# Performance work log

Measured on AMD Instinct MI355X. Metric: run time of the kernel, lower is better.

## Reference

```python
import jax, jax.numpy as jnp
import numpy as np

# Fixed problem sizes (equal-sized batch segments, matching setup_inputs)
B, N, M = 4, 4096, 16384          # clouds, coarse pts/cloud, fine pts/cloud
C_IN, C_SKIP, K = 256, 256, 3     # feature dims, knn k
CH = [C_IN + C_SKIP, 512, 256]    # MLP channels
EPS = 1e-16


def setup_inputs() -> dict:
    key = jax.random.key(0)
    ks = jax.random.split(key, 6)
    x = jax.random.normal(ks[0], (B * N, C_IN), jnp.float32)
    pos = jax.random.uniform(ks[1], (B * N, 3), jnp.float32)
    batch = jnp.repeat(jnp.arange(B, dtype=jnp.int64), N)
    x_skip = jax.random.normal(ks[2], (B * M, C_SKIP), jnp.float32)
    pos_skip = jax.random.uniform(ks[3], (B * M, 3), jnp.float32)
    batch_skip = jnp.repeat(jnp.arange(B, dtype=jnp.int64), M)
    W1 = jax.random.normal(ks[4], (CH[0], CH[1]), jnp.float32) / np.sqrt(CH[0]).astype(np.float32)
    b1 = jnp.zeros((CH[1],), jnp.float32)
    W2 = jax.random.normal(ks[5], (CH[1], CH[2]), jnp.float32) / np.sqrt(CH[1]).astype(np.float32)
    b2 = jnp.zeros((CH[2],), jnp.float32)
    return dict(x=x, pos=pos, batch=batch, x_skip=x_skip, pos_skip=pos_skip,
                batch_skip=batch_skip, W1=W1, b1=b1, W2=W2, b2=b2)


def _knn_interpolate(x, pos, pos_skip):
    """torch_geometric.nn.knn_interpolate with equal-sized batch segments."""
    xb = x.reshape(B, N, C_IN)
    ps = pos.reshape(B, N, 3)
    qs = pos_skip.reshape(B, M, 3)
    # squared pairwise distances [B, M, N]
    d2 = (jnp.sum(qs * qs, -1)[:, :, None]
          - 2.0 * jnp.einsum('bmd,bnd->bmn', qs, ps)
          + jnp.sum(ps * ps, -1)[:, None, :])
    neg_d2, idx = jax.lax.top_k(-d2, K)                # k smallest distances, [B,M,K]
    w = 1.0 / jnp.clip(-neg_d2, EPS)                   # inverse squared distance weights
    feats = jax.vmap(lambda f, i: f[i])(xb, idx)       # gather: [B, M, K, C_IN]
    y = jnp.sum(w[..., None] * feats, axis=2) / jnp.sum(w, axis=2)[..., None]
    return y.reshape(B * M, C_IN)


def reference(x, pos, batch, x_skip, pos_skip, batch_skip, W1, b1, W2, b2):
    y = _knn_interpolate(x, pos, pos_skip)
    h = jnp.concatenate([y, x_skip], axis=1)           # [B*M, 512]
    h = jax.nn.relu(h @ W1 + b1)
    h = jax.nn.relu(h @ W2 + b2)
    return h, pos_skip, batch_skip
```

## Files before the change

### kernel.cpp

```cpp
#include <hip/hip_runtime.h>
#include <stdint.h>

#define NB 4
#define NPTS 4096
#define MPTS 16384
#define CIN 256
#define CH0 512
#define CH1 512
#define CH2 256
#define ROWS (NB * MPTS)
#define POS_OUT_OFF (ROWS * CH2)
#define BATCH_OUT_OFF (POS_OUT_OFF + ROWS * 3)
#define CELL_CAP 40
#define QCAP 96

using u16 = unsigned short;
using u32 = unsigned int;
using u64 = unsigned long long;

typedef __bf16 bf16x8 __attribute__((ext_vector_type(8)));
typedef float f32x4 __attribute__((ext_vector_type(4)));

__device__ __forceinline__ u16 f2bf(float f) {
  u32 u = __builtin_bit_cast(u32, f);
  u32 r = u + 0x7fffu + ((u >> 16) & 1u);
  return (u16)(r >> 16);
}

__device__ __forceinline__ u32 flipf(float f) {
  u32 u = __builtin_bit_cast(u32, f);
  return u ^ ((u32)((int)u >> 31) | 0x80000000u);
}
__device__ __forceinline__ float unflipf(u32 f) {
  u32 m = (~(u32)((int)f >> 31)) | 0x80000000u;
  return __builtin_bit_cast(float, f ^ m);
}

__device__ __forceinline__ void ins3(u64 v, u64& k0, u64& k1, u64& k2) {
  u64 a = k0 < v ? v : k0;
  k0 = k0 < v ? k0 : v;
  u64 bb = k1 < a ? a : k1;
  k1 = k1 < a ? k1 : a;
  k2 = k2 < bb ? k2 : bb;
}

__device__ __forceinline__ void merge3(u64 r0, u64 r1, u64 r2,
                                       u64& k0, u64& k1, u64& k2) {
  u64 t = k0 < r0 ? r0 : k0;
  k0 = k0 < r0 ? k0 : r0;
  u64 u = k1 < r1 ? k1 : r1;
  u64 mtu = t < u ? u : t;
  k1 = t < u ? t : u;
  u64 v = k2 < r2 ? k2 : r2;
  k2 = mtu < v ? mtu : v;
}

__device__ __forceinline__ u64 shfl_xor_u64_w8(u64 v, int mask) {
  u32 lo = (u32)v, hi = (u32)(v >> 32);
  lo = (u32)__shfl_xor((int)lo, mask, 8);
  hi = (u32)__shfl_xor((int)hi, mask, 8);
  return ((u64)hi << 32) | lo;
}

__global__ __launch_bounds__(256) void prep_kernel(
    const float* __restrict__ W1, const float* __restrict__ W2,
    u16* __restrict__ W1s, u16* __restrict__ W2s) {
  const int t = blockIdx.x * 256 + threadIdx.x;
  if (t < 32768) {
    const int l = t & 63, ni = (t >> 6) & 3, wd = (t >> 8) & 7, kt = t >> 11;
    const int fr = l & 15, g = l >> 4;
    const int n = wd * 64 + ni * 16 + fr;
    u16 o[8];
#pragma unroll
    for (int j = 0; j < 8; ++j)
      o[j] = f2bf(W1[(kt * 32 + g * 8 + j) * CH1 + n]);
    *(uint4*)(W1s + (size_t)t * 8) = *(const uint4*)o;
  } else {
    const int c = t - 32768;
    const int l = c & 63, ni = (c >> 6) & 1, wd = (c >> 7) & 7, kt = c >> 10;
    const int fr = l & 15, g = l >> 4;
    const int n = wd * 32 + ni * 16 + fr;
    u16 o[8];
#pragma unroll
    for (int j = 0; j < 8; ++j)
      o[j] = f2bf(W2[(kt * 32 + g * 8 + j) * CH2 + n]);
    *(uint4*)(W2s + (size_t)c * 8) = *(const uint4*)o;
  }
}

__global__ __launch_bounds__(256) void tail_kernel(
    const float* __restrict__ pos_skip, const int* __restrict__ batch_skip,
    float* __restrict__ out) {
  int t = blockIdx.x * 256 + threadIdx.x;
  if (t < ROWS * 3) {
    out[POS_OUT_OFF + t] = pos_skip[t];
  } else {
    int u = t - ROWS * 3;
    out[BATCH_OUT_OFF + u] = (float)batch_skip[u];
  }
}

__global__ __launch_bounds__(256) void build_kernel(
    const float* __restrict__ pos, float4* __restrict__ pts4,
    u32* __restrict__ cellCnt, int* __restrict__ cellIdx) {
#pragma clang fp contract(off)
  const int i = blockIdx.x * 256 + threadIdx.x;
  const float x = pos[i * 3 + 0], y = pos[i * 3 + 1], z = pos[i * 3 + 2];
  pts4[i] = make_float4(x, y, z, (x * x + y * y) + z * z);
  const int b = i >> 12;
  int cx = (int)(x * 8.0f); cx = cx < 0 ? 0 : (cx > 7 ? 7 : cx);
  int cy = (int)(y * 8.0f); cy = cy < 0 ? 0 : (cy > 7 ? 7 : cy);
  int cz = (int)(z * 8.0f); cz = cz < 0 ? 0 : (cz > 7 ? 7 : cz);
  const int c = b * 512 + cz * 64 + cy * 8 + cx;
  const u32 slot = atomicAdd(&cellCnt[c], 1u);
  if (slot < CELL_CAP) cellIdx[c * CELL_CAP + slot] = i;
}

__global__ __launch_bounds__(256) void qbin_kernel(
    const float* __restrict__ pos_skip, u32* __restrict__ qCnt,
    int* __restrict__ qIdx) {
  const int q = blockIdx.x * 256 + threadIdx.x;
  const int b = q >> 14;
  const float qx = pos_skip[q * 3 + 0];
  const float qy = pos_skip[q * 3 + 1];
  const float qz = pos_skip[q * 3 + 2];
  int cx = (int)(qx * 8.0f); cx = cx < 0 ? 0 : (cx > 7 ? 7 : cx);
  int cy = (int)(qy * 8.0f); cy = cy < 0 ? 0 : (cy > 7 ? 7 : cy);
  int cz = (int)(qz * 8.0f); cz = cz < 0 ? 0 : (cz > 7 ? 7 : cz);
  const int c = b * 512 + cz * 64 + cy * 8 + cx;
  const u32 slot = atomicAdd(&qCnt[c], 1u);
  if (slot < QCAP) qIdx[c * QCAP + slot] = q;
}

__global__ __launch_bounds__(256) void knn_kernel(
    const float4* __restrict__ pts4, const u32* __restrict__ cellCnt,
    const int* __restrict__ cellIdx, const u32* __restrict__ qCnt,
    const int* __restrict__ qIdx, const float* __restrict__ pos_skip,
    int* __restrict__ idx_out, float* __restrict__ w_out) {
#pragma clang fp contract(off)
  __shared__ float4 scand[27 * CELL_CAP];
  __shared__ int    scgi[27 * CELL_CAP];
  __shared__ u32    scnt[27];
  __shared__ int    sbase[27];
  __shared__ u32    nCand;
  const int tid = threadIdx.x;
  const int b = blockIdx.x >> 9;
  const int cell = blockIdx.x & 511;
  const int cz = cell >> 6, cy = (cell >> 3) & 7, cx = cell & 7;
  const int x0 = cx > 0 ? cx - 1 : 0, x1 = cx < 7 ? cx + 1 : 7;
  const int y0 = cy > 0 ? cy - 1 : 0, y1 = cy < 7 ? cy + 1 : 7;
  const int z0 = cz > 0 ? cz - 1 : 0, z1 = cz < 7 ? cz + 1 : 7;
  const int nx = x1 - x0 + 1, ny = y1 - y0 + 1, nz = z1 - z0 + 1;
  const int ncells = nx * ny * nz;
  if (tid == 0) nCand = 0;
  if (tid < ncells) {
    const int lz = tid / (nx * ny);
    const int rem = tid - lz * nx * ny;
    const int ly = rem / nx;
    const int lx = rem - ly * nx;
    const int cg = b * 512 + (z0 + lz) * 64 + (y0 + ly) * 8 + (x0 + lx);
    u32 cnt = cellCnt[cg];
    scnt[tid] = cnt > CELL_CAP ? CELL_CAP : cnt;
    sbase[tid] = cg * CELL_CAP;
  }
  __syncthreads();
  const int slots = ncells * CELL_CAP;
  for (int s = tid; s < slots; s += 256) {
    const int ci = s / CELL_CAP;
    const int sl = s - ci * CELL_CAP;
    if ((u32)sl < scnt[ci]) {
      const int gi = cellIdx[sbase[ci] + sl];
      const float4 p = pts4[gi];
      const u32 d = atomicAdd(&nCand, 1u);
      scand[d] = p;
      scgi[d] = gi;
    }
  }
  __syncthreads();
  const int nC = (int)nCand;
  u32 nq = qCnt[b * 512 + cell];
  if (nq > QCAP) nq = QCAP;
  const int qbase = (b * 512 + cell) * QCAP;
  const int g = tid >> 3;
  const int sub = tid & 7;

  for (int r0q = 0; r0q < (int)nq; r0q += 32) {
    const int qslot = r0q + g;
    if (qslot < (int)nq) {
      const int q = qIdx[qbase + qslot];
      const float qx = pos_skip[q * 3 + 0];
      const float qy = pos_skip[q * 3 + 1];
      const float qz = pos_skip[q * 3 + 2];
      const float q2 = (qx * qx + qy * qy) + qz * qz;
      u64 k0 = ~0ull, k1 = ~0ull, k2 = ~0ull;
      for (int s = sub; s < nC; s += 8) {
        const float4 p = scand[s];
        const float dot = fmaf(qz, p.z, fmaf(qy, p.y, qx * p.x));
        const float tv = (q2 - 2.0f * dot) + p.w;
        const u64 key = ((u64)flipf(tv) << 32) | (u32)scgi[s];
        ins3(key, k0, k1, k2);
      }
#pragma unroll
      for (int mask = 1; mask < 8; mask <<= 1) {
        const u64 r0 = shfl_xor_u64_w8(k0, mask);
        const u64 r1 = shfl_xor_u64_w8(k1, mask);
        const u64 r2 = shfl_xor_u64_w8(k2, mask);
        merge3(r0, r1, r2, k0, k1, k2);
      }
      float m2tv = unflipf((u32)(k2 >> 32));
      if (!(m2tv <= 0.015625f - 1e-5f)) {
        k0 = k1 = k2 = ~0ull;
        const int ex0 = cx > 1 ? cx - 2 : 0, ex1 = cx < 6 ? cx + 2 : 7;
        const int ey0 = cy > 1 ? cy - 2 : 0, ey1 = cy < 6 ? cy + 2 : 7;
        const int ez0 = cz > 1 ? cz - 2 : 0, ez1 = cz < 6 ? cz + 2 : 7;
        for (int zz = ez0; zz <= ez1; ++zz)
          for (int yy = ey0; yy <= ey1; ++yy)
            for (int xx = ex0; xx <= ex1; ++xx) {
              const int cg = b * 512 + zz * 64 + yy * 8 + xx;
              u32 cnt = cellCnt[cg];
              if (cnt > CELL_CAP) cnt = CELL_CAP;
              const int cb = cg * CELL_CAP;
              for (int s = sub; s < (int)cnt; s += 8) {
                const int gi = cellIdx[cb + s];
                const float4 p = pts4[gi];
                const float dot = fmaf(qz, p.z, fmaf(qy, p.y, qx * p.x));
                const float tv = (q2 - 2.0f * dot) + p.w;
                ins3(((u64)flipf(tv) << 32) | (u32)gi, k0, k1, k2);
              }
            }
#pragma unroll
        for (int mask = 1; mask < 8; mask <<= 1) {
          const u64 r0 = shfl_xor_u64_w8(k0, mask);
          const u64 r1 = shfl_xor_u64_w8(k1, mask);
          const u64 r2 = shfl_xor_u64_w8(k2, mask);
          merge3(r0, r1, r2, k0, k1, k2);
        }
        m2tv = unflipf((u32)(k2 >> 32));
        if (!(m2tv <= 0.0625f - 1e-5f)) {
          k0 = k1 = k2 = ~0ull;
          const int base = b * NPTS;
          for (int i = sub; i < NPTS; i += 8) {
            const int gi = base + i;
            const float4 p = pts4[gi];
            const float dot = fmaf(qz, p.z, fmaf(qy, p.y, qx * p.x));
            const float tv = (q2 - 2.0f * dot) + p.w;
            ins3(((u64)flipf(tv) << 32) | (u32)gi, k0, k1, k2);
          }
#pragma unroll
          for (int mask = 1; mask < 8; mask <<= 1) {
            const u64 r0 = shfl_xor_u64_w8(k0, mask);
            const u64 r1 = shfl_xor_u64_w8(k1, mask);
            const u64 r2 = shfl_xor_u64_w8(k2, mask);
            merge3(r0, r1, r2, k0, k1, k2);
          }
        }
      }
      if (sub == 0) {
        const float t0 = unflipf((u32)(k0 >> 32));
        const float t1 = unflipf((u32)(k1 >> 32));
        const float t2 = unflipf((u32)(k2 >> 32));
        const float w0 = 1.0f / fmaxf(t0, 1e-16f);
        const float w1 = 1.0f / fmaxf(t1, 1e-16f);
        const float w2 = 1.0f / fmaxf(t2, 1e-16f);
        const float wsum = (w0 + w1) + w2;
        const float inv = 1.0f / wsum;
        idx_out[q * 3 + 0] = (int)(u32)k0;
        idx_out[q * 3 + 1] = (int)(u32)k1;
        idx_out[q * 3 + 2] = (int)(u32)k2;
        w_out[q * 3 + 0] = w0 * inv;
        w_out[q * 3 + 1] = w1 * inv;
        w_out[q * 3 + 2] = w2 * inv;
      }
    }
  }
}

__global__ __launch_bounds__(512, 2) void fused_mlp_kernel(
    const float* __restrict__ x, const int* __restrict__ idx,
    const float* __restrict__ w, const float* __restrict__ x_skip,
    const u16* __restrict__ W1s, const float* __restrict__ b1,
    const u16* __restrict__ W2s, const float* __restrict__ b2,
    float* __restrict__ out) {
  __shared__ __align__(16) u16 Abuf[64 * 512];
  const int tid = threadIdx.x;
  const int m0 = blockIdx.x * 64;

  {
    const int row = tid >> 3;
    const int sub = tid & 7;
    const int gr = m0 + row;
    u16* rowp = Abuf + row * 512;
    const int rx = row & 7;
    if (sub < 4) {
      const int i0 = idx[gr * 3 + 0], i1 = idx[gr * 3 + 1], i2 = idx[gr * 3 + 2];
      const float w0 = w[gr * 3 + 0], w1 = w[gr * 3 + 1], w2 = w[gr * 3 + 2];
      const float4* p0 = (const float4*)(x + (size_t)i0 * CIN + sub * 64);
      const float4* p1 = (const float4*)(x + (size_t)i1 * CIN + sub * 64);
      const float4* p2 = (const float4*)(x + (size_t)i2 * CIN + sub * 64);
#pragma unroll
      for (int c = 0; c < 8; ++c) {
        const float4 a0 = p0[c * 2], a1 = p1[c * 2], a2 = p2[c * 2];
        const float4 d0 = p0[c * 2 + 1], d1 = p1[c * 2 + 1], d2 = p2[c * 2 + 1];
        u16 o[8];
        o[0] = f2bf(fmaf(w0, a0.x, fmaf(w1, a1.x, w2 * a2.x)));
        o[1] = f2bf(fmaf(w0, a0.y, fmaf(w1, a1.y, w2 * a2.y)));
        o[2] = f2bf(fmaf(w0, a0.z, fmaf(w1, a1.z, w2 * a2.z)));
        o[3] = f2bf(fmaf(w0, a0.w, fmaf(w1, a1.w, w2 * a2.w)));
        o[4] = f2bf(fmaf(w0, d0.x, fmaf(w1, d1.x, w2 * d2.x)));
        o[5] = f2bf(fmaf(w0, d0.y, fmaf(w1, d1.y, w2 * d2.y)));
        o[6] = f2bf(fmaf(w0, d0.z, fmaf(w1, d1.z, w2 * d2.z)));
        o[7] = f2bf(fmaf(w0, d0.w, fmaf(w1, d1.w, w2 * d2.w)));
        const int vg = sub * 8 + c;
        *(uint4*)(rowp + (vg ^ rx) * 8) = *(const uint4*)o;
      }
    } else {
      const float4* ps = (const float4*)(x_skip + (size_t)gr * CIN + (sub - 4) * 64);
#pragma unroll
      for (int c = 0; c < 8; ++c) {
        const float4 a = ps[c * 2], d = ps[c * 2 + 1];
        u16 o[8];
        o[0] = f2bf(a.x); o[1] = f2bf(a.y); o[2] = f2bf(a.z); o[3] = f2bf(a.w);
        o[4] = f2bf(d.x); o[5] = f2bf(d.y); o[6] = f2bf(d.z); o[7] = f2bf(d.w);
        const int vg = 32 + (sub - 4) * 8 + c;
        *(uint4*)(rowp + (vg ^ rx) * 8) = *(const uint4*)o;
      }
    }
  }
  __syncthreads();

  const int wid = tid >> 6;
  const int lane = tid & 63;
  const int fr = lane & 15;
  const int g = lane >> 4;
  const int frx = fr & 7;

  f32x4 acc[4][4];
#pragma unroll
  for (int mi = 0; mi < 4; mi++)
#pragma unroll
    for (int ni = 0; ni < 4; ni++) acc[mi][ni] = (f32x4){0.f, 0.f, 0.f, 0.f};

  {
    const u16* B1 = W1s + wid * 2048 + lane * 8;
    bf16x8 bf[2][4];
#pragma unroll
    for (int ni = 0; ni < 4; ni++)
      bf[0][ni] = *(const bf16x8*)(B1 + ni * 512);
    for (int kt = 0; kt < 16; ++kt) {
      const int cur = kt & 1;
      if (kt < 15) {
        const u16* nb = B1 + (kt + 1) * 16384;
#pragma unroll
        for (int ni = 0; ni < 4; ni++)
          bf[cur ^ 1][ni] = *(const bf16x8*)(nb + ni * 512);
      }
      bf16x8 af[4];
#pragma unroll
      for (int mi = 0; mi < 4; mi++)
        af[mi] = *(const bf16x8*)&Abuf[(mi * 16 + fr) * 512 +
                                       (((kt * 4 + g) ^ frx) * 8)];
#pragma unroll
      for (int mi = 0; mi < 4; mi++)
#pragma unroll
        for (int ni = 0; ni < 4; ni++)
          acc[mi][ni] = __builtin_amdgcn_mfma_f32_16x16x32_bf16(
              af[mi], bf[cur][ni], acc[mi][ni], 0, 0, 0);
    }
  }
  __syncthreads();

  {
    const int wn = wid * 64;
#pragma unroll
    for (int ni = 0; ni < 4; ni++) {
      const int n = wn + ni * 16 + fr;
      const float bb = b1[n];
      const int vg = n >> 3;
      const int nlow = n & 7;
#pragma unroll
      for (int mi = 0; mi < 4; mi++) {
#pragma unroll
        for (int r = 0; r < 4; r++) {
          const int m = mi * 16 + g * 4 + r;
          const float v = fmaxf(acc[mi][ni][r] + bb, 0.f);
          Abuf[m * 512 + (vg ^ (m & 7)) * 8 + nlow] = f2bf(v);
        }
      }
    }
  }
  __syncthreads();

  f32x4 acc2[4][2];
#pragma unroll
  for (int mi = 0; mi < 4; mi++)
#pragma unroll
    for (int ni = 0; ni < 2; ni++) acc2[mi][ni] = (f32x4){0.f, 0.f, 0.f, 0.f};

  {
    const u16* B2 = W2s + wid * 1024 + lane * 8;
    bf16x8 bf[2][2];
#pragma unroll
    for (int ni = 0; ni < 2; ni++)
      bf[0][ni] = *(const bf16x8*)(B2 + ni * 512);
    for (int kt = 0; kt < 16; ++kt) {
      const int cur = kt & 1;
      if (kt < 15) {
        const u16* nb = B2 + (kt + 1) * 8192;
#pragma unroll
        for (int ni = 0; ni < 2; ni++)
          bf[cur ^ 1][ni] = *(const bf16x8*)(nb + ni * 512);
      }
      bf16x8 af[4];
#pragma unroll
      for (int mi = 0; mi < 4; mi++)
        af[mi] = *(const bf16x8*)&Abuf[(mi * 16 + fr) * 512 +
                                       (((kt * 4 + g) ^ frx) * 8)];
#pragma unroll
      for (int mi = 0; mi < 4; mi++)
#pragma unroll
        for (int ni = 0; ni < 2; ni++)
          acc2[mi][ni] = __builtin_amdgcn_mfma_f32_16x16x32_bf16(
              af[mi], bf[cur][ni], acc2[mi][ni], 0, 0, 0);
    }
  }

#pragma unroll
  for (int ni = 0; ni < 2; ni++) {
    const int col = wid * 32 + ni * 16 + fr;
    const float bb = b2[col];
#pragma unroll
    for (int mi = 0; mi < 4; mi++) {
#pragma unroll
      for (int r = 0; r < 4; r++) {
        const int rowg = m0 + mi * 16 + g * 4 + r;
        out[(size_t)rowg * CH2 + col] = fmaxf(acc2[mi][ni][r] + bb, 0.f);
      }
    }
  }
}

extern "C" void kernel_launch(void* const* d_in, const int* in_sizes, int n_in,
                              void* d_out, int out_size, void* d_ws, size_t ws_size,
                              hipStream_t stream) {
  const float* x        = (const float*)d_in[0];
  const float* pos      = (const float*)d_in[1];
  const float* x_skip   = (const float*)d_in[3];
  const float* pos_skip = (const float*)d_in[4];
  const int*   batch_sk = (const int*)d_in[5];
  const float* W1       = (const float*)d_in[6];
  const float* b1       = (const float*)d_in[7];
  const float* W2       = (const float*)d_in[8];
  const float* b2       = (const float*)d_in[9];
  float* out = (float*)d_out;

  char* ws = (char*)d_ws;
  u16*    W1s     = (u16*)(ws);
  u16*    W2s     = (u16*)(ws + 524288);
  int*    idxb    = (int*)(ws + 786432);
  float*  wb      = (float*)(ws + 1572864);
  float4* pts4    = (float4*)(ws + 2359296);
  u32*    cellCnt = (u32*)(ws + 2621440);
  u32*    qCnt    = (u32*)(ws + 2629632);
  int*    cellIdx = (int*)(ws + 2637824);
  int*    qIdx    = (int*)(ws + 2965504);

  hipMemsetAsync(cellCnt, 0, 16384, stream);
  prep_kernel<<<dim3(192), dim3(256), 0, stream>>>(W1, W2, W1s, W2s);
  tail_kernel<<<dim3(1024), dim3(256), 0, stream>>>(pos_skip, batch_sk, out);
  build_kernel<<<dim3(64), dim3(256), 0, stream>>>(pos, pts4, cellCnt, cellIdx);
  qbin_kernel<<<dim3(256), dim3(256), 0, stream>>>(pos_skip, qCnt, qIdx);
  knn_kernel<<<dim3(2048), dim3(256), 0, stream>>>(pts4, cellCnt, cellIdx,
                                                   qCnt, qIdx, pos_skip,
                                                   idxb, wb);
  fused_mlp_kernel<<<dim3(1024), dim3(512), 0, stream>>>(
      x, idxb, wb, x_skip, W1s, b1, W2s, b2, out);
}
```

Baseline: 272.0 us.

## Swap MFMA operand roles, split layer-1 N into two passes, raise occupancy

Swaps the MFMA operands so weights are the A operand and activations the B operand. Each lane's accumulator then holds four consecutive output columns, which allows packed 8-byte LDS stores for the hidden layer and float4 global stores for the output. Layer 1 now runs in two passes of half the N width, with the first pass's bf16 results packed into registers. This cuts accumulator registers so launch bounds can rise to 4 blocks per CU. The cost is re-reading the A tiles from LDS in each pass, and occupancy is still capped by the 64 KB shared buffer per block.

New measurement: 280.8 us. 3.2% more time.

```diff
diff --git a/kernel.cpp b/kernel.cpp
--- a/kernel.cpp
+++ b/kernel.cpp
@@ -275,7 +275,7 @@
   }
 }
 
-__global__ __launch_bounds__(512, 2) void fused_mlp_kernel(
+__global__ __launch_bounds__(512, 4) void fused_mlp_kernel(
     const float* __restrict__ x, const int* __restrict__ idx,
     const float* __restrict__ w, const float* __restrict__ x_skip,
     const u16* __restrict__ W1s, const float* __restrict__ b1,
@@ -334,107 +334,133 @@
   const int g = lane >> 4;
   const int frx = fr & 7;
 
-  f32x4 acc[4][4];
-#pragma unroll
-  for (int mi = 0; mi < 4; mi++)
-#pragma unroll
-    for (int ni = 0; ni < 4; ni++) acc[mi][ni] = (f32x4){0.f, 0.f, 0.f, 0.f};
-
-  {
-    const u16* B1 = W1s + wid * 2048 + lane * 8;
-    bf16x8 bf[2][4];
-#pragma unroll
-    for (int ni = 0; ni < 4; ni++)
-      bf[0][ni] = *(const bf16x8*)(B1 + ni * 512);
+  f32x4 acc[2][4];
+  u32 hold[16];
+#pragma unroll
+  for (int p = 0; p < 2; ++p) {
+#pragma unroll
+    for (int mi = 0; mi < 2; mi++)
+#pragma unroll
+      for (int ni = 0; ni < 4; ni++) acc[mi][ni] = (f32x4){0.f, 0.f, 0.f, 0.f};
+    const u16* B1 = W1s + wid * 2048 + (p * 2) * 512 + lane * 8;
+    bf16x8 bw[2][2];
+#pragma unroll
+    for (int i = 0; i < 2; i++) bw[0][i] = *(const bf16x8*)(B1 + i * 512);
     for (int kt = 0; kt < 16; ++kt) {
       const int cur = kt & 1;
       if (kt < 15) {
         const u16* nb = B1 + (kt + 1) * 16384;
 #pragma unroll
-        for (int ni = 0; ni < 4; ni++)
-          bf[cur ^ 1][ni] = *(const bf16x8*)(nb + ni * 512);
+        for (int i = 0; i < 2; i++)
+          bw[cur ^ 1][i] = *(const bf16x8*)(nb + i * 512);
       }
       bf16x8 af[4];
 #pragma unroll
-      for (int mi = 0; mi < 4; mi++)
-        af[mi] = *(const bf16x8*)&Abuf[(mi * 16 + fr) * 512 +
+      for (int ni = 0; ni < 4; ni++)
+        af[ni] = *(const bf16x8*)&Abuf[(ni * 16 + fr) * 512 +
                                        (((kt * 4 + g) ^ frx) * 8)];
 #pragma unroll
-      for (int mi = 0; mi < 4; mi++)
+      for (int mi = 0; mi < 2; mi++)
 #pragma unroll
         for (int ni = 0; ni < 4; ni++)
           acc[mi][ni] = __builtin_amdgcn_mfma_f32_16x16x32_bf16(
-              af[mi], bf[cur][ni], acc[mi][ni], 0, 0, 0);
+              bw[cur][mi], af[ni], acc[mi][ni], 0, 0, 0);
+    }
+    if (p == 0) {
+#pragma unroll
+      for (int mi = 0; mi < 2; mi++) {
+        const int cb = wid * 64 + mi * 16 + g * 4;
+        const float4 bv = *(const float4*)&b1[cb];
+#pragma unroll
+        for (int ni = 0; ni < 4; ni++) {
+          const u16 t0 = f2bf(fmaxf(acc[mi][ni][0] + bv.x, 0.f));
+          const u16 t1 = f2bf(fmaxf(acc[mi][ni][1] + bv.y, 0.f));
+          const u16 t2 = f2bf(fmaxf(acc[mi][ni][2] + bv.z, 0.f));
+          const u16 t3 = f2bf(fmaxf(acc[mi][ni][3] + bv.w, 0.f));
+          hold[(mi * 4 + ni) * 2 + 0] = (u32)t0 | ((u32)t1 << 16);
+          hold[(mi * 4 + ni) * 2 + 1] = (u32)t2 | ((u32)t3 << 16);
+        }
+      }
     }
   }
   __syncthreads();
 
-  {
-    const int wn = wid * 64;
-#pragma unroll
-    for (int ni = 0; ni < 4; ni++) {
-      const int n = wn + ni * 16 + fr;
-      const float bb = b1[n];
-      const int vg = n >> 3;
-      const int nlow = n & 7;
-#pragma unroll
-      for (int mi = 0; mi < 4; mi++) {
-#pragma unroll
-        for (int r = 0; r < 4; r++) {
-          const int m = mi * 16 + g * 4 + r;
-          const float v = fmaxf(acc[mi][ni][r] + bb, 0.f);
-          Abuf[m * 512 + (vg ^ (m & 7)) * 8 + nlow] = f2bf(v);
-        }
+#pragma unroll
+  for (int mi = 0; mi < 2; mi++) {
+    {
+      const int cb = wid * 64 + mi * 16 + g * 4;
+      const int vg = cb >> 3, cl = cb & 7;
+#pragma unroll
+      for (int ni = 0; ni < 4; ni++) {
+        const int row = ni * 16 + fr;
+        uint2 pk = make_uint2(hold[(mi * 4 + ni) * 2 + 0],
+                              hold[(mi * 4 + ni) * 2 + 1]);
+        *(uint2*)&Abuf[row * 512 + (vg ^ (row & 7)) * 8 + cl] = pk;
+      }
+    }
+    {
+      const int cb = wid * 64 + 32 + mi * 16 + g * 4;
+      const float4 bv = *(const float4*)&b1[cb];
+      const int vg = cb >> 3, cl = cb & 7;
+#pragma unroll
+      for (int ni = 0; ni < 4; ni++) {
+        const int row = ni * 16 + fr;
+        uint2 pk;
+        pk.x = (u32)f2bf(fmaxf(acc[mi][ni][0] + bv.x, 0.f)) |
+               ((u32)f2bf(fmaxf(acc[mi][ni][1] + bv.y, 0.f)) << 16);
+        pk.y = (u32)f2bf(fmaxf(acc[mi][ni][2] + bv.z, 0.f)) |
+               ((u32)f2bf(fmaxf(acc[mi][ni][3] + bv.w, 0.f)) << 16);
+        *(uint2*)&Abuf[row * 512 + (vg ^ (row & 7)) * 8 + cl] = pk;
       }
     }
   }
   __syncthreads();
 
-  f32x4 acc2[4][2];
-#pragma unroll
-  for (int mi = 0; mi < 4; mi++)
-#pragma unroll
-    for (int ni = 0; ni < 2; ni++) acc2[mi][ni] = (f32x4){0.f, 0.f, 0.f, 0.f};
-
+  f32x4 acc2[2][4];
+#pragma unroll
+  for (int mi = 0; mi < 2; mi++)
+#pragma unroll
+    for (int ni = 0; ni < 4; ni++) acc2[mi][ni] = (f32x4){0.f, 0.f, 0.f, 0.f};
   {
     const u16* B2 = W2s + wid * 1024 + lane * 8;
-    bf16x8 bf[2][2];
-#pragma unroll
-    for (int ni = 0; ni < 2; ni++)
-      bf[0][ni] = *(const bf16x8*)(B2 + ni * 512);
+    bf16x8 bw[2][2];
+#pragma unroll
+    for (int i = 0; i < 2; i++) bw[0][i] = *(const bf16x8*)(B2 + i * 512);
     for (int kt = 0; kt < 16; ++kt) {
       const int cur = kt & 1;
       if (kt < 15) {
         const u16* nb = B2 + (kt + 1) * 8192;
 #pragma unroll
-        for (int ni = 0; ni < 2; ni++)
-          bf[cur ^ 1][ni] = *(const bf16x8*)(nb + ni * 512);
+        for (int i = 0; i < 2; i++)
+          bw[cur ^ 1][i] = *(const bf16x8*)(nb + i * 512);
       }
       bf16x8 af[4];
 #pragma unroll
-      for (int mi = 0; mi < 4; mi++)
-        af[mi] = *(const bf16x8*)&Abuf[(mi * 16 + fr) * 512 +
+      for (int ni = 0; ni < 4; ni++)
+        af[ni] = *(const bf16x8*)&Abuf[(ni * 16 + fr) * 512 +
                                        (((kt * 4 + g) ^ frx) * 8)];
 #pragma unroll
-      for (int mi = 0; mi < 4; mi++)
-#pragma unroll
-        for (int ni = 0; ni < 2; ni++)
+      for (int mi = 0; mi < 2; mi++)
+#pragma unroll
+        for (int ni = 0; ni < 4; ni++)
           acc2[mi][ni] = __builtin_amdgcn_mfma_f32_16x16x32_bf16(
-              af[mi], bf[cur][ni], acc2[mi][ni], 0, 0, 0);
-    }
-  }
-
-#pragma unroll
-  for (int ni = 0; ni < 2; ni++) {
-    const int col = wid * 32 + ni * 16 + fr;
-    const float bb = b2[col];
-#pragma unroll
-    for (int mi = 0; mi < 4; mi++) {
-#pragma unroll
-      for (int r = 0; r < 4; r++) {
-        const int rowg = m0 + mi * 16 + g * 4 + r;
-        out[(size_t)rowg * CH2 + col] = fmaxf(acc2[mi][ni][r] + bb, 0.f);
-      }
+              bw[cur][mi], af[ni], acc2[mi][ni], 0, 0, 0);
+    }
+  }
+
+#pragma unroll
+  for (int mi = 0; mi < 2; mi++) {
+    const int cb = wid * 32 + mi * 16 + g * 4;
+    const float4 bv = *(const float4*)&b2[cb];
+#pragma unroll
+    for (int ni = 0; ni < 4; ni++) {
+      const int row = m0 + ni * 16 + fr;
+      float4 o;
+      o.x = fmaxf(acc2[mi][ni][0] + bv.x, 0.f);
+      o.y = fmaxf(acc2[mi][ni][1] + bv.y, 0.f);
+      o.z = fmaxf(acc2[mi][ni][2] + bv.z, 0.f);
+      o.w = fmaxf(acc2[mi][ni][3] + bv.w, 0.f);
+      *(float4*)&out[(size_t)row * CH2 + cb] = o;
     }
   }
 }
```
